# Kernel tuning notes

Hardware: AMD Instinct MI355X
Metric: run time of the kernel (lower is better)

## Reference

```python
import jax, jax.numpy as jnp
import numpy as np

EMBED_DIM = 1024
NUM_HEADS = 16
HEAD_DIM = EMBED_DIM // NUM_HEADS
SCALING = HEAD_DIM ** -0.5
NEG_FILL = -1e30


def setup_inputs() -> dict:
    key = jax.random.key(0)
    k1, k2, k3 = jax.random.split(key, 3)
    T, B, E = 2048, 4, EMBED_DIM
    query = jax.random.normal(k1, (T, B, E), dtype=jnp.float32)
    key_padding_mask = jnp.zeros((B, T), dtype=bool)  # 1 = padded key
    # xavier_uniform-like init
    lim_in = (6.0 / (3 * E + E)) ** 0.5
    in_proj_weight = jax.random.uniform(k2, (3 * E, E), minval=-lim_in, maxval=lim_in, dtype=jnp.float32)
    in_proj_bias = jnp.zeros((3 * E,), dtype=jnp.float32)
    lim_out = (6.0 / (E + E)) ** 0.5
    out_w = jax.random.uniform(k3, (E, E), minval=-lim_out, maxval=lim_out, dtype=jnp.float32)
    out_b = jnp.zeros((E,), dtype=jnp.float32)
    return {"query": query, "key_padding_mask": key_padding_mask,
            "in_proj_weight": in_proj_weight, "in_proj_bias": in_proj_bias,
            "out_w": out_w, "out_b": out_b}


def reference(query, key_padding_mask, in_proj_weight, in_proj_bias, out_w, out_b):
    T, B, E = query.shape
    H, D = NUM_HEADS, HEAD_DIM
    # fused in-projection (self-attention: qkv from same input)
    qkv = query @ in_proj_weight.T + in_proj_bias  # [T,B,3E]
    q, k, v = jnp.split(qkv, 3, axis=-1)
    q = q * SCALING
    q = q.reshape(T, B, H, D)
    k = k.reshape(T, B, H, D)
    v = v.reshape(T, B, H, D)
    # attention scores [B,H,T,S]
    scores = jnp.einsum('tbhd,sbhd->bhts', q, k)
    scores = jnp.where(key_padding_mask[:, None, None, :], NEG_FILL, scores)
    attn_w = jax.nn.softmax(scores, axis=-1)  # [B,H,T,S]
    # weighted sum of values -> [T,B,E]
    attn = jnp.einsum('bhts,sbhd->tbhd', attn_w, v).reshape(T, B, E)
    attn = attn @ out_w.T + out_b
    attn_w_avg = jnp.sum(attn_w, axis=1) / H  # [B,T,S]
    return attn, attn_w_avg
```

## Files before the change

kernel.cpp:

```cpp
#include <hip/hip_runtime.h>
#include <stdint.h>

#define LOG2E 1.44269504088896340736f
#define QSCALE 0.18033688011112042f

typedef unsigned short u16;
typedef __attribute__((ext_vector_type(8))) __bf16 bf16x8;
typedef __attribute__((ext_vector_type(4))) __bf16 bf16x4;
typedef __attribute__((ext_vector_type(4))) float f32x4;
typedef __attribute__((ext_vector_type(8))) u16 u16x8;

__device__ __forceinline__ void gl_lds16(const void* g, void* l) {
  __builtin_amdgcn_global_load_lds(
      (const __attribute__((address_space(1))) void*)g,
      (__attribute__((address_space(3))) void*)l, 16, 0, 0);
}

__device__ __forceinline__ u16 f2bf(float f) {
  unsigned int u = __float_as_uint(f);
  u += 0x7FFFu + ((u >> 16) & 1u);
  return (u16)(u >> 16);
}

extern "C" __global__ __launch_bounds__(256) void cvt_f32_bf16(
    const float* __restrict__ src, u16* __restrict__ dst, int n) {
  int i = (blockIdx.x * 256 + threadIdx.x) * 4;
  if (i >= n) return;
  float4 v = *(const float4*)(src + i);
  ushort4 o;
  o.x = f2bf(v.x); o.y = f2bf(v.y); o.z = f2bf(v.z); o.w = f2bf(v.w);
  *(ushort4*)(dst + i) = o;
}

extern "C" __global__ __launch_bounds__(256) void gemm_qkv(
    const u16* __restrict__ X, const u16* __restrict__ W,
    const float* __restrict__ bias,
    u16* __restrict__ qb, u16* __restrict__ kb, u16* __restrict__ vb) {
  const int tid = threadIdx.x;
  const int w = tid >> 6, lane = tid & 63;
  const int lg = lane >> 4, ll = lane & 15;
  const int wm = w >> 1, wn = w & 1;
  const int row0A = blockIdx.x * 128;
  const int row0B = blockIdx.y * 128;

  __shared__ __align__(16) u16 As[2][128 * 32];
  __shared__ __align__(16) u16 Bs[2][128 * 32];

  f32x4 acc[4][4] = {};

  const int r_st = tid >> 2;
  const int cb_st = (tid & 3) * 16;

#pragma unroll
  for (int it = 0; it < 2; ++it) {
    gl_lds16((const char*)X + ((size_t)(row0A + it * 64 + r_st) * 1024) * 2 + cb_st,
             (char*)&As[0][0] + it * 4096 + w * 1024);
    gl_lds16((const char*)W + ((size_t)(row0B + it * 64 + r_st) * 1024) * 2 + cb_st,
             (char*)&Bs[0][0] + it * 4096 + w * 1024);
  }

  for (int kt = 0; kt < 32; ++kt) {
    const int cur = kt & 1;
    asm volatile("s_waitcnt vmcnt(0)" ::: "memory");
    __syncthreads();
    if (kt + 1 < 32) {
      const int k0 = (kt + 1) * 32;
#pragma unroll
      for (int it = 0; it < 2; ++it) {
        gl_lds16((const char*)X + ((size_t)(row0A + it * 64 + r_st) * 1024 + k0) * 2 + cb_st,
                 (char*)&As[cur ^ 1][0] + it * 4096 + w * 1024);
        gl_lds16((const char*)W + ((size_t)(row0B + it * 64 + r_st) * 1024 + k0) * 2 + cb_st,
                 (char*)&Bs[cur ^ 1][0] + it * 4096 + w * 1024);
      }
    }
    const u16* Ab = &As[cur][0];
    const u16* Bb = &Bs[cur][0];
    const int kc = lg * 8;
    bf16x8 a[4], bfr[4];
#pragma unroll
    for (int i = 0; i < 4; ++i)
      a[i] = *(const bf16x8*)(Ab + (wm * 64 + i * 16 + ll) * 32 + kc);
#pragma unroll
    for (int j = 0; j < 4; ++j)
      bfr[j] = *(const bf16x8*)(Bb + (wn * 64 + j * 16 + ll) * 32 + kc);
#pragma unroll
    for (int i = 0; i < 4; ++i)
#pragma unroll
      for (int j = 0; j < 4; ++j)
        acc[i][j] = __builtin_amdgcn_mfma_f32_16x16x32_bf16(a[i], bfr[j], acc[i][j], 0, 0, 0);
  }

  const int which = row0B >> 10;
  u16* dst = which == 0 ? qb : (which == 1 ? kb : vb);
  const float scl = which == 0 ? QSCALE : 1.0f;
#pragma unroll
  for (int j = 0; j < 4; ++j) {
    const int n = row0B + wn * 64 + j * 16 + ll;
    const float bv = bias[n];
    const int n2 = n & 1023;
    const int hh = n2 >> 6, dd = n2 & 63;
#pragma unroll
    for (int i = 0; i < 4; ++i)
#pragma unroll
      for (int r = 0; r < 4; ++r) {
        const int m = row0A + wm * 64 + i * 16 + lg * 4 + r;
        const int tt = m >> 2, bb = m & 3;
        dst[((size_t)(bb * 16 + hh) * 2048 + tt) * 64 + dd] = f2bf((acc[i][j][r] + bv) * scl);
      }
  }
}

extern "C" __global__ __launch_bounds__(256) void transpose_v(
    const u16* __restrict__ v, u16* __restrict__ vt) {
  const int blk = blockIdx.x;
  const int bh = blk >> 5, tt = blk & 31;
  const int t0 = tt * 64;
  const int tid = threadIdx.x;
  __shared__ __align__(16) u16 tile[64][72];
  const u16* src = v + ((size_t)bh * 2048 + t0) * 64;
#pragma unroll
  for (int it = 0; it < 2; ++it) {
    const int r = it * 32 + (tid >> 3);
    const int c = (tid & 7) * 8;
    *(u16x8*)(&tile[r][c]) = *(const u16x8*)(src + (size_t)r * 64 + c);
  }
  __syncthreads();
  u16* dstb = vt + (size_t)bh * 64 * 2048 + t0;
#pragma unroll
  for (int it = 0; it < 2; ++it) {
    const int d = it * 32 + (tid >> 3);
    const int s = (tid & 7) * 8;
    u16x8 o;
#pragma unroll
    for (int jj = 0; jj < 8; ++jj) o[jj] = tile[s + jj][d];
    *(u16x8*)(dstb + (size_t)d * 2048 + s) = o;
  }
}

extern "C" __global__ __launch_bounds__(256, 4) void flash_fwd(
    const u16* __restrict__ q, const u16* __restrict__ k,
    const u16* __restrict__ vt, const unsigned char* __restrict__ mask,
    u16* __restrict__ attn_pre, float* __restrict__ stat_il) {
  const int blk = blockIdx.x;
  const int bh = blk >> 5, tt = blk & 31;
  const int b = bh >> 4, h = bh & 15;
  const int t0 = tt * 64;
  const int tid = threadIdx.x, w = tid >> 6, lane = tid & 63;
  const int lg = lane >> 4, ll = lane & 15;
  const int x7 = ll & 7;

  __shared__ __align__(16) u16 Ks[2][64 * 64];
  __shared__ __align__(16) u16 Vs[2][64 * 64];
  __shared__ __align__(16) u16 Ps[4][16 * 64];

  const int qrow = t0 + w * 16 + ll;
  const u16* qp = q + ((size_t)bh * 2048 + qrow) * 64 + lg * 8;
  const bf16x8 aq0 = *(const bf16x8*)(qp);
  const bf16x8 aq1 = *(const bf16x8*)(qp + 32);

  f32x4 po[4] = {};
  float lsum = 0.f;

  const int slot_r = tid >> 3;
  const int slot_c8 = (tid & 7) ^ (slot_r & 7);
  const unsigned char* mrow = mask + b * 2048 + lg * 4;
  u16* pw = &Ps[w][0];

  const int ko0 = (lg ^ x7) << 3;
  const int ko1 = ((4 + lg) ^ x7) << 3;

#define STAGE_F(buf, s0_)                                                      \
  do {                                                                         \
    _Pragma("unroll") for (int it2 = 0; it2 < 2; ++it2) {                      \
      const int rr = it2 * 32 + slot_r;                                        \
      gl_lds16((const char*)k +                                                \
                   (((size_t)bh * 2048 + (s0_) + rr) * 64 + slot_c8 * 8) * 2,  \
               (char*)&Ks[buf][0] + it2 * 4096 + w * 1024);                    \
      gl_lds16((const char*)vt +                                               \
                   (((size_t)bh * 64 + rr) * 2048 + (s0_) + slot_c8 * 8) * 2,  \
               (char*)&Vs[buf][0] + it2 * 4096 + w * 1024);                    \
    }                                                                          \
  } while (0)

  STAGE_F(0, 0);
  asm volatile("s_waitcnt vmcnt(0)" ::: "memory");
  __syncthreads();

  for (int it = 0; it < 32; ++it) {
    const int s0 = it * 64;
    const int cur = it & 1;

    unsigned mq[4];
#pragma unroll
    for (int j = 0; j < 4; ++j)
      mq[j] = *(const unsigned*)(mrow + s0 + j * 16);

    if (it + 1 < 32) STAGE_F(cur ^ 1, s0 + 64);

    const u16* Kb = &Ks[cur][0];
    const u16* Vb = &Vs[cur][0];

    f32x4 z[4];
#pragma unroll
    for (int j = 0; j < 4; ++j) {
      const int krow = j * 16 + ll;
      const bf16x8 kb0 = *(const bf16x8*)(Kb + krow * 64 + ko0);
      const bf16x8 kb1 = *(const bf16x8*)(Kb + krow * 64 + ko1);
      f32x4 zz = {};
      zz = __builtin_amdgcn_mfma_f32_16x16x32_bf16(kb0, aq0, zz, 0, 0, 0);
      zz = __builtin_amdgcn_mfma_f32_16x16x32_bf16(kb1, aq1, zz, 0, 0, 0);
      z[j] = zz;
    }

#pragma unroll
    for (int j = 0; j < 4; ++j) {
      bf16x4 pk;
#pragma unroll
      for (int r = 0; r < 4; ++r) {
        float p = __builtin_amdgcn_exp2f(z[j][r]);
        p = (mq[j] & (0xFFu << (r * 8))) ? 0.f : p;
        lsum += p;
        pk[r] = (__bf16)p;
      }
      const int c8 = j * 2 + (lg >> 1);
      *(bf16x4*)(pw + ll * 64 + ((c8 ^ x7) << 3) + (lg & 1) * 4) = pk;
    }

#pragma unroll
    for (int kk = 0; kk < 2; ++kk) {
      const bf16x8 pa =
          *(const bf16x8*)(pw + ll * 64 + (((kk * 4 + lg) ^ x7) << 3));
      const int vo = ((kk * 4 + lg) ^ x7) << 3;
#pragma unroll
      for (int j = 0; j < 4; ++j) {
        const bf16x8 bv = *(const bf16x8*)(Vb + (j * 16 + ll) * 64 + vo);
        po[j] = __builtin_amdgcn_mfma_f32_16x16x32_bf16(pa, bv, po[j], 0, 0, 0);
      }
    }

    asm volatile("s_waitcnt vmcnt(0)" ::: "memory");
    __syncthreads();
  }

  lsum += __shfl_xor(lsum, 16, 64);
  lsum += __shfl_xor(lsum, 32, 64);
  const float linv = 1.0f / lsum;
  if (lane < 16)
    stat_il[(size_t)bh * 2048 + t0 + w * 16 + ll] = linv;
  float il[4];
#pragma unroll
  for (int r = 0; r < 4; ++r) il[r] = __shfl(linv, lg * 4 + r, 64);
#pragma unroll
  for (int j = 0; j < 4; ++j) {
    const int dd = j * 16 + ll;
#pragma unroll
    for (int r = 0; r < 4; ++r) {
      const int trow = t0 + w * 16 + lg * 4 + r;
      attn_pre[((size_t)(trow * 4 + b)) * 1024 + h * 64 + dd] =
          f2bf(po[j][r] * il[r]);
    }
  }
#undef STAGE_F
}

extern "C" __global__ __launch_bounds__(256, 4) void wavg(
    const u16* __restrict__ q, const u16* __restrict__ k,
    const unsigned char* __restrict__ mask,
    const float* __restrict__ stat_il, float* __restrict__ wout) {
  const int blk = blockIdx.x;
  const int b = blk >> 10, tt = (blk >> 5) & 31, st = blk & 31;
  const int t0 = tt * 64, s0 = st * 64;
  const int tid = threadIdx.x, w = tid >> 6, lane = tid & 63;
  const int lg = lane >> 4, ll = lane & 15;
  const int x7 = ll & 7;

  __shared__ __align__(16) u16 Qs[2][64 * 64];
  __shared__ __align__(16) u16 Ks2[2][64 * 64];

  const int slot_r = tid >> 3;
  const int slot_c8 = (tid & 7) ^ (slot_r & 7);

  bool msk[4];
#pragma unroll
  for (int j = 0; j < 4; ++j) msk[j] = mask[b * 2048 + s0 + j * 16 + ll] != 0;

  const int ko0 = (lg ^ x7) << 3;
  const int ko1 = ((4 + lg) ^ x7) << 3;

#define STAGE_W(buf, hh)                                                       \
  do {                                                                         \
    const size_t qo_ = (size_t)(b * 16 + (hh)) * 2048;                         \
    _Pragma("unroll") for (int it2 = 0; it2 < 2; ++it2) {                      \
      const int rr = it2 * 32 + slot_r;                                        \
      gl_lds16((const char*)q + ((qo_ + t0 + rr) * 64 + slot_c8 * 8) * 2,      \
               (char*)&Qs[buf][0] + it2 * 4096 + w * 1024);                    \
      gl_lds16((const char*)k + ((qo_ + s0 + rr) * 64 + slot_c8 * 8) * 2,      \
               (char*)&Ks2[buf][0] + it2 * 4096 + w * 1024);                   \
    }                                                                          \
  } while (0)

  STAGE_W(0, 0);
  asm volatile("s_waitcnt vmcnt(0)" ::: "memory");
  __syncthreads();

  float accw[4][4] = {};
  for (int h = 0; h < 16; ++h) {
    const int cur = h & 1;
    const size_t qoff = (size_t)(b * 16 + h) * 2048;

    float ilh[4];
#pragma unroll
    for (int r = 0; r < 4; ++r)
      ilh[r] = stat_il[qoff + t0 + w * 16 + lg * 4 + r];

    if (h + 1 < 16) STAGE_W(cur ^ 1, h + 1);

    const u16* Qb = &Qs[cur][0];
    const u16* Kb = &Ks2[cur][0];
    const int qr = w * 16 + ll;
    const bf16x8 a0 = *(const bf16x8*)(Qb + qr * 64 + ko0);
    const bf16x8 a1 = *(const bf16x8*)(Qb + qr * 64 + ko1);

#pragma unroll
    for (int j = 0; j < 4; ++j) {
      const int krow = j * 16 + ll;
      const bf16x8 b0 = *(const bf16x8*)(Kb + krow * 64 + ko0);
      const bf16x8 b1 = *(const bf16x8*)(Kb + krow * 64 + ko1);
      f32x4 z = {};
      z = __builtin_amdgcn_mfma_f32_16x16x32_bf16(a0, b0, z, 0, 0, 0);
      z = __builtin_amdgcn_mfma_f32_16x16x32_bf16(a1, b1, z, 0, 0, 0);
#pragma unroll
      for (int r = 0; r < 4; ++r) {
        float p = msk[j] ? 0.f : __builtin_amdgcn_exp2f(z[r]);
        accw[j][r] = fmaf(p, ilh[r], accw[j][r]);
      }
    }

    asm volatile("s_waitcnt vmcnt(0)" ::: "memory");
    __syncthreads();
  }

#pragma unroll
  for (int j = 0; j < 4; ++j) {
    const int scol = s0 + j * 16 + ll;
#pragma unroll
    for (int r = 0; r < 4; ++r) {
      const int trow = t0 + w * 16 + lg * 4 + r;
      wout[((size_t)b * 2048 + trow) * 2048 + scol] = accw[j][r] * 0.0625f;
    }
  }
#undef STAGE_W
}

extern "C" __global__ __launch_bounds__(256) void gemm_out(
    const u16* __restrict__ A, const u16* __restrict__ W,
    const float* __restrict__ bias, float* __restrict__ out) {
  const int tid = threadIdx.x;
  const int w = tid >> 6, lane = tid & 63;
  const int lg = lane >> 4, ll = lane & 15;
  const int wm = w >> 1, wn = w & 1;
  const int row0A = blockIdx.x * 128;
  const int row0B = blockIdx.y * 128;

  __shared__ __align__(16) u16 As[2][128 * 32];
  __shared__ __align__(16) u16 Bs[2][128 * 32];

  f32x4 acc[4][4] = {};
  const int r_st = tid >> 2;
  const int cb_st = (tid & 3) * 16;

#pragma unroll
  for (int it = 0; it < 2; ++it) {
    gl_lds16((const char*)A + ((size_t)(row0A + it * 64 + r_st) * 1024) * 2 + cb_st,
             (char*)&As[0][0] + it * 4096 + w * 1024);
    gl_lds16((const char*)W + ((size_t)(row0B + it * 64 + r_st) * 1024) * 2 + cb_st,
             (char*)&Bs[0][0] + it * 4096 + w * 1024);
  }

  for (int kt = 0; kt < 32; ++kt) {
    const int cur = kt & 1;
    asm volatile("s_waitcnt vmcnt(0)" ::: "memory");
    __syncthreads();
    if (kt + 1 < 32) {
      const int k0 = (kt + 1) * 32;
#pragma unroll
      for (int it = 0; it < 2; ++it) {
        gl_lds16((const char*)A + ((size_t)(row0A + it * 64 + r_st) * 1024 + k0) * 2 + cb_st,
                 (char*)&As[cur ^ 1][0] + it * 4096 + w * 1024);
        gl_lds16((const char*)W + ((size_t)(row0B + it * 64 + r_st) * 1024 + k0) * 2 + cb_st,
                 (char*)&Bs[cur ^ 1][0] + it * 4096 + w * 1024);
      }
    }
    const u16* Ab = &As[cur][0];
    const u16* Bb = &Bs[cur][0];
    const int kc = lg * 8;
    bf16x8 a[4], bfr[4];
#pragma unroll
    for (int i = 0; i < 4; ++i)
      a[i] = *(const bf16x8*)(Ab + (wm * 64 + i * 16 + ll) * 32 + kc);
#pragma unroll
    for (int j = 0; j < 4; ++j)
      bfr[j] = *(const bf16x8*)(Bb + (wn * 64 + j * 16 + ll) * 32 + kc);
#pragma unroll
    for (int i = 0; i < 4; ++i)
#pragma unroll
      for (int j = 0; j < 4; ++j)
        acc[i][j] = __builtin_amdgcn_mfma_f32_16x16x32_bf16(a[i], bfr[j], acc[i][j], 0, 0, 0);
  }

#pragma unroll
  for (int j = 0; j < 4; ++j) {
    const int n = row0B + wn * 64 + j * 16 + ll;
    const float bv = bias[n];
#pragma unroll
    for (int i = 0; i < 4; ++i)
#pragma unroll
      for (int r = 0; r < 4; ++r) {
        const int m = row0A + wm * 64 + i * 16 + lg * 4 + r;
        out[(size_t)m * 1024 + n] = acc[i][j][r] + bv;
      }
  }
}

extern "C" void kernel_launch(void* const* d_in, const int* in_sizes, int n_in,
                              void* d_out, int out_size, void* d_ws, size_t ws_size,
                              hipStream_t stream) {
  const float* query = (const float*)d_in[0];
  const unsigned char* mask = (const unsigned char*)d_in[1];
  const float* w_in = (const float*)d_in[2];
  const float* b_in = (const float*)d_in[3];
  const float* w_out = (const float*)d_in[4];
  const float* b_out = (const float*)d_in[5];

  float* out0 = (float*)d_out;
  float* outw = out0 + (size_t)8388608;

  char* ws = (char*)d_ws;
  u16* Xbf   = (u16*)(ws + 0);
  u16* Wqkv  = (u16*)(ws + 16777216);
  u16* Woutb = (u16*)(ws + 23068672);
  u16* qb    = (u16*)(ws + 25165824);
  u16* kb    = (u16*)(ws + 41943040);
  u16* vb    = (u16*)(ws + 58720256);
  u16* vtb   = (u16*)(ws + 75497472);
  u16* ap    = (u16*)(ws + 92274688);
  float* sil = (float*)(ws + 109051904);

  cvt_f32_bf16<<<8192, 256, 0, stream>>>(query, Xbf, 8388608);
  cvt_f32_bf16<<<3072, 256, 0, stream>>>(w_in, Wqkv, 3145728);
  cvt_f32_bf16<<<1024, 256, 0, stream>>>(w_out, Woutb, 1048576);
  gemm_qkv<<<dim3(64, 24), 256, 0, stream>>>(Xbf, Wqkv, b_in, qb, kb, vb);
  transpose_v<<<2048, 256, 0, stream>>>(vb, vtb);
  flash_fwd<<<2048, 256, 0, stream>>>(qb, kb, vtb, mask, ap, sil);
  wavg<<<4096, 256, 0, stream>>>(qb, kb, mask, sil, outw);
  gemm_out<<<dim3(64, 8), 256, 0, stream>>>(ap, Woutb, b_out, out0);
}
```

Baseline: 321.5 us.

## Switch attention kernels to 32x32x16 MFMA with 128-row query tiles

flash_fwd and wavg move from 16x16x32 to 32x32x16 bf16 MFMA, with each wave owning 32 query rows and each block 128 rows, which halves the grid sizes. In flash_fwd the P matrix stays in registers and is reshuffled with v_permlane32_swap, removing the LDS round trip for P. Mask application is skipped when a wave-wide check finds no padded keys. wavg now writes its fp32 output through an LDS-swizzled transpose so global stores are full 16-byte row-contiguous vectors; it also drops to 3 waves-per-SIMD occupancy because of the larger Q buffer and accumulator.

```diff
diff --git a/kernel.cpp b/kernel.cpp
--- a/kernel.cpp
+++ b/kernel.cpp
@@ -1,14 +1,15 @@
 #include <hip/hip_runtime.h>
 #include <stdint.h>
 
-#define LOG2E 1.44269504088896340736f
 #define QSCALE 0.18033688011112042f
 
 typedef unsigned short u16;
+typedef unsigned int u32;
 typedef __attribute__((ext_vector_type(8))) __bf16 bf16x8;
-typedef __attribute__((ext_vector_type(4))) __bf16 bf16x4;
 typedef __attribute__((ext_vector_type(4))) float f32x4;
+typedef __attribute__((ext_vector_type(16))) float f32x16;
 typedef __attribute__((ext_vector_type(8))) u16 u16x8;
+typedef __attribute__((ext_vector_type(4))) u32 u32x4;
 
 __device__ __forceinline__ void gl_lds16(const void* g, void* l) {
   __builtin_amdgcn_global_load_lds(
@@ -20,6 +21,10 @@
   unsigned int u = __float_as_uint(f);
   u += 0x7FFFu + ((u >> 16) & 1u);
   return (u16)(u >> 16);
+}
+
+__device__ __forceinline__ u32 pk2(float a, float b) {
+  return (u32)f2bf(a) | ((u32)f2bf(b) << 16);
 }
 
 extern "C" __global__ __launch_bounds__(256) void cvt_f32_bf16(
@@ -142,32 +147,28 @@
     const u16* __restrict__ vt, const unsigned char* __restrict__ mask,
     u16* __restrict__ attn_pre, float* __restrict__ stat_il) {
   const int blk = blockIdx.x;
-  const int bh = blk >> 5, tt = blk & 31;
-  const int b = bh >> 4, h = bh & 15;
-  const int t0 = tt * 64;
+  const int bh = blk >> 4, tt = blk & 15;
+  const int b = bh >> 4, hd = bh & 15;
+  const int t0 = tt * 128;
   const int tid = threadIdx.x, w = tid >> 6, lane = tid & 63;
-  const int lg = lane >> 4, ll = lane & 15;
-  const int x7 = ll & 7;
+  const int hl = lane >> 5;
+  const int l31 = lane & 31;
 
   __shared__ __align__(16) u16 Ks[2][64 * 64];
   __shared__ __align__(16) u16 Vs[2][64 * 64];
-  __shared__ __align__(16) u16 Ps[4][16 * 64];
-
-  const int qrow = t0 + w * 16 + ll;
-  const u16* qp = q + ((size_t)bh * 2048 + qrow) * 64 + lg * 8;
-  const bf16x8 aq0 = *(const bf16x8*)(qp);
-  const bf16x8 aq1 = *(const bf16x8*)(qp + 32);
-
-  f32x4 po[4] = {};
+
+  const int qrow = t0 + w * 32 + l31;
+  const u16* qp = q + ((size_t)bh * 2048 + qrow) * 64 + hl * 8;
+  bf16x8 qreg[4];
+#pragma unroll
+  for (int kg = 0; kg < 4; ++kg) qreg[kg] = *(const bf16x8*)(qp + kg * 16);
+
+  f32x16 po[2] = {};
   float lsum = 0.f;
 
   const int slot_r = tid >> 3;
   const int slot_c8 = (tid & 7) ^ (slot_r & 7);
-  const unsigned char* mrow = mask + b * 2048 + lg * 4;
-  u16* pw = &Ps[w][0];
-
-  const int ko0 = (lg ^ x7) << 3;
-  const int ko1 = ((4 + lg) ^ x7) << 3;
+  const unsigned char* mrow = mask + b * 2048 + hl * 4;
 
 #define STAGE_F(buf, s0_)                                                      \
   do {                                                                         \
@@ -190,51 +191,63 @@
     const int s0 = it * 64;
     const int cur = it & 1;
 
-    unsigned mq[4];
-#pragma unroll
-    for (int j = 0; j < 4; ++j)
-      mq[j] = *(const unsigned*)(mrow + s0 + j * 16);
+    u32 mq[8];
+#pragma unroll
+    for (int kt = 0; kt < 2; ++kt)
+#pragma unroll
+      for (int j = 0; j < 4; ++j)
+        mq[kt * 4 + j] = *(const u32*)(mrow + s0 + kt * 32 + j * 8);
+    const u32 anym = mq[0] | mq[1] | mq[2] | mq[3] | mq[4] | mq[5] | mq[6] | mq[7];
 
     if (it + 1 < 32) STAGE_F(cur ^ 1, s0 + 64);
 
-    const u16* Kb = &Ks[cur][0];
-    const u16* Vb = &Vs[cur][0];
-
-    f32x4 z[4];
-#pragma unroll
-    for (int j = 0; j < 4; ++j) {
-      const int krow = j * 16 + ll;
-      const bf16x8 kb0 = *(const bf16x8*)(Kb + krow * 64 + ko0);
-      const bf16x8 kb1 = *(const bf16x8*)(Kb + krow * 64 + ko1);
-      f32x4 zz = {};
-      zz = __builtin_amdgcn_mfma_f32_16x16x32_bf16(kb0, aq0, zz, 0, 0, 0);
-      zz = __builtin_amdgcn_mfma_f32_16x16x32_bf16(kb1, aq1, zz, 0, 0, 0);
-      z[j] = zz;
-    }
-
-#pragma unroll
-    for (int j = 0; j < 4; ++j) {
-      bf16x4 pk;
-#pragma unroll
-      for (int r = 0; r < 4; ++r) {
-        float p = __builtin_amdgcn_exp2f(z[j][r]);
-        p = (mq[j] & (0xFFu << (r * 8))) ? 0.f : p;
-        lsum += p;
-        pk[r] = (__bf16)p;
-      }
-      const int c8 = j * 2 + (lg >> 1);
-      *(bf16x4*)(pw + ll * 64 + ((c8 ^ x7) << 3) + (lg & 1) * 4) = pk;
-    }
-
-#pragma unroll
-    for (int kk = 0; kk < 2; ++kk) {
-      const bf16x8 pa =
-          *(const bf16x8*)(pw + ll * 64 + (((kk * 4 + lg) ^ x7) << 3));
-      const int vo = ((kk * 4 + lg) ^ x7) << 3;
+    const char* Kb = (const char*)&Ks[cur][0];
+    const char* Vb = (const char*)&Vs[cur][0];
+
+#pragma unroll
+    for (int kt = 0; kt < 2; ++kt) {
+      f32x16 z = {};
+      const int key = kt * 32 + l31;
+#pragma unroll
+      for (int kg = 0; kg < 4; ++kg) {
+        const bf16x8 kf = *(const bf16x8*)(
+            Kb + key * 128 + ((((kg << 1) | hl) ^ (key & 7)) << 4));
+        z = __builtin_amdgcn_mfma_f32_32x32x16_bf16(kf, qreg[kg], z, 0, 0, 0);
+      }
+
+      float ps[16];
+#pragma unroll
+      for (int r = 0; r < 16; ++r) ps[r] = __builtin_amdgcn_exp2f(z[r]);
+      if (__any(anym != 0)) {
+#pragma unroll
+        for (int r = 0; r < 16; ++r)
+          if ((mq[kt * 4 + (r >> 2)] >> ((r & 3) * 8)) & 0xFFu) ps[r] = 0.f;
+      }
+#pragma unroll
+      for (int r = 0; r < 16; ++r) lsum += ps[r];
+
+      u32 w8[8];
 #pragma unroll
       for (int j = 0; j < 4; ++j) {
-        const bf16x8 bv = *(const bf16x8*)(Vb + (j * 16 + ll) * 64 + vo);
-        po[j] = __builtin_amdgcn_mfma_f32_16x16x32_bf16(pa, bv, po[j], 0, 0, 0);
+        w8[2 * j] = pk2(ps[4 * j], ps[4 * j + 1]);
+        w8[2 * j + 1] = pk2(ps[4 * j + 2], ps[4 * j + 3]);
+      }
+
+#pragma unroll
+      for (int f = 0; f < 2; ++f) {
+        u32 d0 = w8[4 * f], d1 = w8[4 * f + 1];
+        u32 s0w = w8[4 * f + 2], s1w = w8[4 * f + 3];
+        asm volatile("v_permlane32_swap_b32 %0, %1" : "+v"(d0), "+v"(s0w));
+        asm volatile("v_permlane32_swap_b32 %0, %1" : "+v"(d1), "+v"(s1w));
+        const bf16x8 pa = __builtin_bit_cast(bf16x8, (u32x4){d0, d1, s0w, s1w});
+        const int g = kt * 2 + f;
+#pragma unroll
+        for (int dt = 0; dt < 2; ++dt) {
+          const int d = dt * 32 + l31;
+          const bf16x8 vf = *(const bf16x8*)(
+              Vb + d * 128 + ((((g << 1) | hl) ^ (d & 7)) << 4));
+          po[dt] = __builtin_amdgcn_mfma_f32_32x32x16_bf16(pa, vf, po[dt], 0, 0, 0);
+        }
       }
     }
 
@@ -242,60 +255,64 @@
     __syncthreads();
   }
 
-  lsum += __shfl_xor(lsum, 16, 64);
   lsum += __shfl_xor(lsum, 32, 64);
   const float linv = 1.0f / lsum;
-  if (lane < 16)
-    stat_il[(size_t)bh * 2048 + t0 + w * 16 + ll] = linv;
-  float il[4];
-#pragma unroll
-  for (int r = 0; r < 4; ++r) il[r] = __shfl(linv, lg * 4 + r, 64);
-#pragma unroll
-  for (int j = 0; j < 4; ++j) {
-    const int dd = j * 16 + ll;
-#pragma unroll
-    for (int r = 0; r < 4; ++r) {
-      const int trow = t0 + w * 16 + lg * 4 + r;
-      attn_pre[((size_t)(trow * 4 + b)) * 1024 + h * 64 + dd] =
-          f2bf(po[j][r] * il[r]);
+  if (lane < 32)
+    stat_il[(size_t)bh * 2048 + t0 + w * 32 + lane] = linv;
+
+#pragma unroll
+  for (int r = 0; r < 16; ++r) {
+    const int qi = (r & 3) + 8 * (r >> 2) + 4 * hl;
+    const float lv = __shfl(linv, qi, 64);
+    const int trow = t0 + w * 32 + qi;
+#pragma unroll
+    for (int dt = 0; dt < 2; ++dt) {
+      const int dd = dt * 32 + l31;
+      attn_pre[((size_t)(trow * 4 + b)) * 1024 + hd * 64 + dd] =
+          f2bf(po[dt][r] * lv);
     }
   }
 #undef STAGE_F
 }
 
-extern "C" __global__ __launch_bounds__(256, 4) void wavg(
+extern "C" __global__ __launch_bounds__(256, 3) void wavg(
     const u16* __restrict__ q, const u16* __restrict__ k,
     const unsigned char* __restrict__ mask,
     const float* __restrict__ stat_il, float* __restrict__ wout) {
   const int blk = blockIdx.x;
-  const int b = blk >> 10, tt = (blk >> 5) & 31, st = blk & 31;
-  const int t0 = tt * 64, s0 = st * 64;
+  const int b = blk >> 9, tt = (blk >> 5) & 15, st = blk & 31;
+  const int t0 = tt * 128, s0 = st * 64;
   const int tid = threadIdx.x, w = tid >> 6, lane = tid & 63;
-  const int lg = lane >> 4, ll = lane & 15;
-  const int x7 = ll & 7;
-
-  __shared__ __align__(16) u16 Qs[2][64 * 64];
+  const int hl = lane >> 5;
+  const int l31 = lane & 31;
+
+  __shared__ __align__(16) u16 Qs[2][128 * 64];
   __shared__ __align__(16) u16 Ks2[2][64 * 64];
 
-  const int slot_r = tid >> 3;
-  const int slot_c8 = (tid & 7) ^ (slot_r & 7);
-
-  bool msk[4];
-#pragma unroll
-  for (int j = 0; j < 4; ++j) msk[j] = mask[b * 2048 + s0 + j * 16 + ll] != 0;
-
-  const int ko0 = (lg ^ x7) << 3;
-  const int ko1 = ((4 + lg) ^ x7) << 3;
+  const int slot_r8 = tid >> 3;
+  const int slot_c8 = (tid & 7) ^ (slot_r8 & 7);
+
+  u32 mq[8];
+#pragma unroll
+  for (int kt = 0; kt < 2; ++kt)
+#pragma unroll
+    for (int j = 0; j < 4; ++j)
+      mq[kt * 4 + j] = *(const u32*)(mask + b * 2048 + s0 + kt * 32 + j * 8 + hl * 4);
+  const u32 anym = mq[0] | mq[1] | mq[2] | mq[3] | mq[4] | mq[5] | mq[6] | mq[7];
+  const bool domask = __any(anym != 0);
 
 #define STAGE_W(buf, hh)                                                       \
   do {                                                                         \
     const size_t qo_ = (size_t)(b * 16 + (hh)) * 2048;                         \
-    _Pragma("unroll") for (int it2 = 0; it2 < 2; ++it2) {                      \
-      const int rr = it2 * 32 + slot_r;                                        \
+    _Pragma("unroll") for (int i2 = 0; i2 < 4; ++i2) {                         \
+      const int rr = i2 * 32 + slot_r8;                                        \
       gl_lds16((const char*)q + ((qo_ + t0 + rr) * 64 + slot_c8 * 8) * 2,      \
-               (char*)&Qs[buf][0] + it2 * 4096 + w * 1024);                    \
+               (char*)&Qs[buf][0] + i2 * 4096 + w * 1024);                     \
+    }                                                                          \
+    _Pragma("unroll") for (int i2 = 0; i2 < 2; ++i2) {                         \
+      const int rr = i2 * 32 + slot_r8;                                        \
       gl_lds16((const char*)k + ((qo_ + s0 + rr) * 64 + slot_c8 * 8) * 2,      \
-               (char*)&Ks2[buf][0] + it2 * 4096 + w * 1024);                   \
+               (char*)&Ks2[buf][0] + i2 * 4096 + w * 1024);                    \
     }                                                                          \
   } while (0)
 
@@ -303,51 +320,70 @@
   asm volatile("s_waitcnt vmcnt(0)" ::: "memory");
   __syncthreads();
 
-  float accw[4][4] = {};
+  float accw[32] = {};
   for (int h = 0; h < 16; ++h) {
     const int cur = h & 1;
-    const size_t qoff = (size_t)(b * 16 + h) * 2048;
-
-    float ilh[4];
-#pragma unroll
-    for (int r = 0; r < 4; ++r)
-      ilh[r] = stat_il[qoff + t0 + w * 16 + lg * 4 + r];
+    const float ilh =
+        stat_il[(size_t)(b * 16 + h) * 2048 + t0 + w * 32 + l31];
 
     if (h + 1 < 16) STAGE_W(cur ^ 1, h + 1);
 
-    const u16* Qb = &Qs[cur][0];
-    const u16* Kb = &Ks2[cur][0];
-    const int qr = w * 16 + ll;
-    const bf16x8 a0 = *(const bf16x8*)(Qb + qr * 64 + ko0);
-    const bf16x8 a1 = *(const bf16x8*)(Qb + qr * 64 + ko1);
-
-#pragma unroll
-    for (int j = 0; j < 4; ++j) {
-      const int krow = j * 16 + ll;
-      const bf16x8 b0 = *(const bf16x8*)(Kb + krow * 64 + ko0);
-      const bf16x8 b1 = *(const bf16x8*)(Kb + krow * 64 + ko1);
-      f32x4 z = {};
-      z = __builtin_amdgcn_mfma_f32_16x16x32_bf16(a0, b0, z, 0, 0, 0);
-      z = __builtin_amdgcn_mfma_f32_16x16x32_bf16(a1, b1, z, 0, 0, 0);
-#pragma unroll
-      for (int r = 0; r < 4; ++r) {
-        float p = msk[j] ? 0.f : __builtin_amdgcn_exp2f(z[r]);
-        accw[j][r] = fmaf(p, ilh[r], accw[j][r]);
-      }
+    const char* Qb = (const char*)&Qs[cur][0];
+    const char* Kb = (const char*)&Ks2[cur][0];
+
+    const int qr = w * 32 + l31;
+    bf16x8 qf[4];
+#pragma unroll
+    for (int kg = 0; kg < 4; ++kg)
+      qf[kg] = *(const bf16x8*)(
+          Qb + qr * 128 + ((((kg << 1) | hl) ^ (qr & 7)) << 4));
+
+#pragma unroll
+    for (int kt = 0; kt < 2; ++kt) {
+      f32x16 z = {};
+      const int key = kt * 32 + l31;
+#pragma unroll
+      for (int kg = 0; kg < 4; ++kg) {
+        const bf16x8 kf = *(const bf16x8*)(
+            Kb + key * 128 + ((((kg << 1) | hl) ^ (key & 7)) << 4));
+        z = __builtin_amdgcn_mfma_f32_32x32x16_bf16(kf, qf[kg], z, 0, 0, 0);
+      }
+      float ps[16];
+#pragma unroll
+      for (int r = 0; r < 16; ++r) ps[r] = __builtin_amdgcn_exp2f(z[r]);
+      if (domask) {
+#pragma unroll
+        for (int r = 0; r < 16; ++r)
+          if ((mq[kt * 4 + (r >> 2)] >> ((r & 3) * 8)) & 0xFFu) ps[r] = 0.f;
+      }
+#pragma unroll
+      for (int r = 0; r < 16; ++r)
+        accw[kt * 16 + r] = fmaf(ps[r], ilh, accw[kt * 16 + r]);
     }
 
     asm volatile("s_waitcnt vmcnt(0)" ::: "memory");
     __syncthreads();
   }
 
-#pragma unroll
-  for (int j = 0; j < 4; ++j) {
-    const int scol = s0 + j * 16 + ll;
-#pragma unroll
-    for (int r = 0; r < 4; ++r) {
-      const int trow = t0 + w * 16 + lg * 4 + r;
-      wout[((size_t)b * 2048 + trow) * 2048 + scol] = accw[j][r] * 0.0625f;
-    }
+  float* tb = ((float*)&Qs[0][0]) + w * 2048;
+#pragma unroll
+  for (int kt = 0; kt < 2; ++kt)
+#pragma unroll
+    for (int j = 0; j < 4; ++j) {
+      f32x4 qd;
+#pragma unroll
+      for (int e = 0; e < 4; ++e) qd[e] = accw[kt * 16 + 4 * j + e] * 0.0625f;
+      const int slot = kt * 8 + 2 * j + hl;
+      *(f32x4*)(tb + l31 * 64 + ((slot ^ (l31 & 7)) << 2)) = qd;
+    }
+  __syncthreads();
+#pragma unroll
+  for (int j2 = 0; j2 < 8; ++j2) {
+    const int row = j2 * 4 + (lane >> 4);
+    const int slot = lane & 15;
+    const f32x4 v = *(const f32x4*)(tb + row * 64 + ((slot ^ (row & 7)) << 2));
+    *(f32x4*)(wout + ((size_t)b * 2048 + t0 + w * 32 + row) * 2048 + s0 +
+              slot * 4) = v;
   }
 #undef STAGE_W
 }
@@ -451,7 +487,7 @@
   cvt_f32_bf16<<<1024, 256, 0, stream>>>(w_out, Woutb, 1048576);
   gemm_qkv<<<dim3(64, 24), 256, 0, stream>>>(Xbf, Wqkv, b_in, qb, kb, vb);
   transpose_v<<<2048, 256, 0, stream>>>(vb, vtb);
-  flash_fwd<<<2048, 256, 0, stream>>>(qb, kb, vtb, mask, ap, sil);
-  wavg<<<4096, 256, 0, stream>>>(qb, kb, mask, sil, outw);
+  flash_fwd<<<1024, 256, 0, stream>>>(qb, kb, vtb, mask, ap, sil);
+  wavg<<<2048, 256, 0, stream>>>(qb, kb, mask, sil, outw);
   gemm_out<<<dim3(64, 8), 256, 0, stream>>>(ap, Woutb, b_out, out0);
 }
```

New measurement: 292.5 us. 9.0% less time.
